# Optimization experiments

Hardware: AMD Instinct MI355X
Metric: run time of the kernel (lower is better)

## Reference

```python
import jax, jax.numpy as jnp
import numpy as np


def setup_inputs() -> dict:
    key = jax.random.key(0)
    k1, _ = jax.random.split(key)
    x = jax.random.normal(k1, (2, 16, 16, 16, 64), dtype=jnp.float32)
    gamma = jnp.ones((1,), dtype=jnp.float32)  # learned scalar (zeros at init; ones to make output nontrivial)
    return {"x": x, "gamma": gamma}


def reference(x, gamma):
    # x: (B, D, H, W, C); faithful to the Keras layer: flatten spatial dims,
    # energy = Q @ Q^T over the N=D*H*W axis, softmax(axis=-1), attn @ Q,
    # then gamma-scaled residual add.
    B, D, H, W, C = x.shape
    N = D * H * W
    q = x.reshape(B, N, C)                            # proj_query (B, N, C)
    energy = jnp.einsum('bnc,bmc->bnm', q, q)          # (B, N, N)
    attn = jax.nn.softmax(energy, axis=-1)
    out = jnp.einsum('bnm,bmc->bnc', attn, q)          # (B, N, C)
    out = out.reshape(B, D, H, W, C)
    return gamma * out + x
```

## Files before the change

### kernel.cpp

```cpp
#include <hip/hip_runtime.h>
#include <hip/hip_bf16.h>
#include <math.h>


#define NN 4096
#define CC 64
#define LOG2E 1.4426950408889634f

typedef __attribute__((ext_vector_type(4))) float f32x4;
typedef __attribute__((ext_vector_type(8))) short bf16x8;
typedef __attribute__((ext_vector_type(4))) short bf16x4;
typedef unsigned short u16;
typedef __attribute__((ext_vector_type(4))) u16 u16x4;

__device__ inline u16 f2bf(float f) {
  union { float f; unsigned u; } v; v.f = f;
  unsigned r = (v.u + 0x7fffu + ((v.u >> 16) & 1u)) >> 16;
  return (u16)r;
}
__device__ inline u16 f2bf_t(float f) {
  union { float f; unsigned u; } v; v.f = f;
  return (u16)(v.u >> 16);
}
__device__ inline float bf2f(short h) {
  union { unsigned u; float f; } v;
  v.u = ((unsigned)(unsigned short)h) << 16;
  return v.f;
}
__device__ inline bf16x8 cvt8(f32x4 a, f32x4 b) {
  bf16x8 r;
  r[0] = (short)f2bf(a[0]); r[1] = (short)f2bf(a[1]);
  r[2] = (short)f2bf(a[2]); r[3] = (short)f2bf(a[3]);
  r[4] = (short)f2bf(b[0]); r[5] = (short)f2bf(b[1]);
  r[6] = (short)f2bf(b[2]); r[7] = (short)f2bf(b[3]);
  return r;
}

__global__ __launch_bounds__(256) void prep_kernel(const float* __restrict__ x,
                                                   u16* __restrict__ Qb,
                                                   u16* __restrict__ Vt) {
  __shared__ u16 t[64][20];
  int b = blockIdx.x >> 8;
  int n0 = (blockIdx.x & 255) << 4;
  const f32x4* x4 = (const f32x4*)(x + ((size_t)b * NN + n0) * CC);
  u16* qb = Qb + ((size_t)b * NN + n0) * CC;
  {
    int idx4 = threadIdx.x;
    int i = idx4 >> 4, cg = idx4 & 15;
    f32x4 v = x4[idx4];
    u16x4 h;
    h[0] = f2bf(v[0]); h[1] = f2bf(v[1]); h[2] = f2bf(v[2]); h[3] = f2bf(v[3]);
    *(u16x4*)(qb + (size_t)i * CC + cg * 4) = h;
    t[cg * 4 + 0][i] = h[0]; t[cg * 4 + 1][i] = h[1];
    t[cg * 4 + 2][i] = h[2]; t[cg * 4 + 3][i] = h[3];
  }
  __syncthreads();
  int kb = n0 >> 6, kw0 = n0 & 63;
  {
    int idx4 = threadIdx.x;
    int c = idx4 >> 2, i4 = (idx4 & 3) * 4;
    u16x4 h = *(const u16x4*)(&t[c][i4]);
    *(u16x4*)(Vt + (((size_t)b * (NN / 64) + kb) * 64 + c) * 64 + kw0 + i4) = h;
  }
}

template <int S>
__global__ __launch_bounds__(256, 2) void attn_split(
    const u16* __restrict__ Qb, const u16* __restrict__ Vt,
    u16* __restrict__ Opart, float* __restrict__ lpart) {
  constexpr int KPS = NN / S;
  constexpr int ITERS = KPS / 64;
  const int w = threadIdx.x >> 6;
  const int lane = threadIdx.x & 63;
  const int quad = lane >> 4, col = lane & 15;
  const int blk = blockIdx.x;
  const int b = blk / (32 * S);
  const int rb = (blk / S) & 31;
  const int s = blk % S;

  __shared__ u16 KT[2][64 * 68];
  __shared__ u16 VT[2][64 * 68];
  __shared__ u16 PB[4][16 * 68];

  const u16* Qbase = Qb + (size_t)b * NN * CC;
  const u16* Vbase = Vt + (size_t)b * NN * CC;
  const int row0 = rb * 128 + w * 32;

  bf16x8 qs0[2], qs1[2];
  float m_i[2][4];
#pragma unroll
  for (int rt = 0; rt < 2; ++rt) {
    const u16* qp = Qbase + (size_t)(row0 + rt * 16 + col) * CC + quad * 8;
    bf16x8 r0 = *(const bf16x8*)qp;
    bf16x8 r1 = *(const bf16x8*)(qp + 32);
    float msum = 0.f;
#pragma unroll
    for (int j = 0; j < 8; ++j) {
      float a0 = bf2f(r0[j]), a1 = bf2f(r1[j]);
      u16 h0 = f2bf(a0 * LOG2E), h1 = f2bf(a1 * LOG2E);
      qs0[rt][j] = (short)h0; qs1[rt][j] = (short)h1;
      msum += bf2f((short)h0) * a0 + bf2f((short)h1) * a1;
    }
    msum += __shfl_xor(msum, 16);
    msum += __shfl_xor(msum, 32);
#pragma unroll
    for (int r = 0; r < 4; ++r) m_i[rt][r] = __shfl(msum, quad * 4 + r);
  }

  f32x4 zero = {0.f, 0.f, 0.f, 0.f};
  f32x4 acc[2][4] = {{zero, zero, zero, zero}, {zero, zero, zero, zero}};
  float l_i[2][4] = {{0.f, 0.f, 0.f, 0.f}, {0.f, 0.f, 0.f, 0.f}};

  const int srow = w * 16 + (lane >> 3);
  const int sj = lane & 7;
  bf16x8 stK0, stK1, stV0, stV1;

  auto issue_loads = [&](int kt0) {
    const u16* ks = Qbase + (size_t)(kt0 + srow) * CC + sj * 8;
    stK0 = *(const bf16x8*)ks;
    stK1 = *(const bf16x8*)(ks + 8 * CC);
    const u16* vs = Vbase + ((size_t)(kt0 >> 6)) * 4096 + srow * 64 + sj * 8;
    stV0 = *(const bf16x8*)vs;
    stV1 = *(const bf16x8*)(vs + 8 * 64);
  };
  auto write_tile = [&](int p) {
    *(bf16x8*)(&KT[p][srow * 68 + sj * 8]) = stK0;
    *(bf16x8*)(&KT[p][(srow + 8) * 68 + sj * 8]) = stK1;
    *(bf16x8*)(&VT[p][srow * 68 + sj * 8]) = stV0;
    *(bf16x8*)(&VT[p][(srow + 8) * 68 + sj * 8]) = stV1;
  };

  issue_loads(s * KPS);
  write_tile(0);
#pragma unroll
  for (int i = 0; i < ITERS; ++i) {
    __syncthreads();
    const int p = i & 1;
    if (i + 1 < ITERS) issue_loads(s * KPS + (i + 1) * 64);
    bf16x8 ka[4], kb_[4], va[4], vb[4];
#pragma unroll
    for (int t = 0; t < 4; ++t) {
      ka[t] = *(const bf16x8*)(&KT[p][(t * 16 + col) * 68 + quad * 8]);
      kb_[t] = *(const bf16x8*)(&KT[p][(t * 16 + col) * 68 + 32 + quad * 8]);
      va[t] = *(const bf16x8*)(&VT[p][(t * 16 + col) * 68 + quad * 8]);
      vb[t] = *(const bf16x8*)(&VT[p][(t * 16 + col) * 68 + 32 + quad * 8]);
    }
#pragma unroll
    for (int rt = 0; rt < 2; ++rt) {
      f32x4 sx[4];
#pragma unroll
      for (int t = 0; t < 4; ++t) {
        sx[t] = __builtin_amdgcn_mfma_f32_16x16x32_bf16(qs0[rt], ka[t], zero, 0, 0, 0);
        sx[t] = __builtin_amdgcn_mfma_f32_16x16x32_bf16(qs1[rt], kb_[t], sx[t], 0, 0, 0);
      }
#pragma unroll
      for (int t = 0; t < 4; ++t) {
#pragma unroll
        for (int r = 0; r < 4; ++r) {
          float pv = exp2f(sx[t][r] - m_i[rt][r]);
          l_i[rt][r] += pv;
          PB[w][(quad * 4 + r) * 68 + t * 16 + col] = f2bf_t(pv);
        }
      }
      bf16x8 pf0 = *(const bf16x8*)(&PB[w][col * 68 + quad * 8]);
      bf16x8 pf1 = *(const bf16x8*)(&PB[w][col * 68 + 32 + quad * 8]);
#pragma unroll
      for (int cg = 0; cg < 4; ++cg) {
        acc[rt][cg] = __builtin_amdgcn_mfma_f32_16x16x32_bf16(pf0, va[cg], acc[rt][cg], 0, 0, 0);
        acc[rt][cg] = __builtin_amdgcn_mfma_f32_16x16x32_bf16(pf1, vb[cg], acc[rt][cg], 0, 0, 0);
      }
    }
    if (i + 1 < ITERS) write_tile(p ^ 1);
  }

#pragma unroll
  for (int rt = 0; rt < 2; ++rt)
#pragma unroll
    for (int r = 0; r < 4; ++r)
#pragma unroll
      for (int off = 1; off < 16; off <<= 1)
        l_i[rt][r] += __shfl_xor(l_i[rt][r], off, 16);

  size_t pbase = (((size_t)b * 32 + rb) * S + s) * 128 * 64;
#pragma unroll
  for (int rt = 0; rt < 2; ++rt) {
#pragma unroll
    for (int r = 0; r < 4; ++r) {
      int lr = w * 32 + rt * 16 + quad * 4 + r;
      size_t o = pbase + (size_t)lr * 64;
      Opart[o + col]      = f2bf(acc[rt][0][r]);
      Opart[o + col + 16] = f2bf(acc[rt][1][r]);
      Opart[o + col + 32] = f2bf(acc[rt][2][r]);
      Opart[o + col + 48] = f2bf(acc[rt][3][r]);
      if (col == 0)
        lpart[(((size_t)b * 32 + rb) * S + s) * 128 + lr] = l_i[rt][r];
    }
  }
}

template <int S>
__global__ __launch_bounds__(256) void epi_kernel(
    const float* __restrict__ x, const float* __restrict__ gamma,
    const u16* __restrict__ Opart, const float* __restrict__ lpart,
    float* __restrict__ out) {
  int t = blockIdx.x * 256 + threadIdx.x;
  int cg = t & 15;
  int n = (t >> 4) & (NN - 1);
  int b = t >> 16;
  int rb = n >> 7, lr = n & 127;
  size_t obase = (((size_t)b * 32 + rb) * S) * 128 * 64 + (size_t)lr * 64 + cg * 4;
  size_t lbase = (((size_t)b * 32 + rb) * S) * 128 + lr;
  f32x4 sO = {0.f, 0.f, 0.f, 0.f};
  float sL = 0.f;
#pragma unroll
  for (int s = 0; s < S; ++s) {
    u16x4 o4 = *(const u16x4*)(Opart + obase + (size_t)s * 128 * 64);
    sL += lpart[lbase + s * 128];
    sO[0] += bf2f((short)o4[0]); sO[1] += bf2f((short)o4[1]);
    sO[2] += bf2f((short)o4[2]); sO[3] += bf2f((short)o4[3]);
  }
  size_t xi = (((size_t)b * NN + n) * CC + cg * 4);
  f32x4 xv = *(const f32x4*)(x + xi);
  float g = gamma[0], inv = 1.f / sL;
  f32x4 ov;
#pragma unroll
  for (int j = 0; j < 4; ++j) ov[j] = g * (sO[j] * inv) + xv[j];
  *(f32x4*)(((float*)out) + xi) = ov;
}

template <int WPB>
__global__ __launch_bounds__(WPB * 64, 4) void attn_fast(
    const float* __restrict__ x, const float* __restrict__ gamma,
    const u16* __restrict__ Qb, const u16* __restrict__ Vt,
    float* __restrict__ out) {
  const int w = threadIdx.x >> 6;
  const int lane = threadIdx.x & 63;
  const int quad = lane >> 4, col = lane & 15;
  const int b = blockIdx.x >> 8;
  const int tile = (blockIdx.x & 255) << 4;

  extern __shared__ char smem[];
  float* Osh = (float*)smem;
  float* lsh = Osh + WPB * 1024;
  u16* pl = (u16*)(lsh + WPB * 16) + w * 2176;

  const size_t xoff = (size_t)b * NN * CC;
  const u16* Qbase = Qb + xoff;
  const u16* Vbase = Vt + xoff;

  bf16x8 qf0 = *(const bf16x8*)(Qbase + (size_t)(tile + col) * CC + quad * 8);
  bf16x8 qf1 = *(const bf16x8*)(Qbase + (size_t)(tile + col) * CC + 32 + quad * 8);

  float msum = 0.f;
#pragma unroll
  for (int j = 0; j < 8; ++j) {
    float a = bf2f(qf0[j]), c = bf2f(qf1[j]);
    msum += a * a + c * c;
  }
  msum += __shfl_xor(msum, 16);
  msum += __shfl_xor(msum, 32);
  float m_i[4];
#pragma unroll
  for (int r = 0; r < 4; ++r) m_i[r] = __shfl(msum, quad * 4 + r);

  f32x4 zero = {0.f, 0.f, 0.f, 0.f};
  f32x4 acc[4] = {zero, zero, zero, zero};
  float l_i[4] = {0.f, 0.f, 0.f, 0.f};

  const int k0 = w * (NN / WPB);
#pragma unroll 2
  for (int kt = k0; kt < k0 + NN / WPB; kt += 64) {
    u16* plc = pl + ((kt >> 6) & 1) * 1088;
    f32x4 sx[4];
#pragma unroll
    for (int t = 0; t < 4; ++t) {
      const u16* kp = Qbase + (size_t)(kt + t * 16 + col) * CC + quad * 8;
      bf16x8 ka = *(const bf16x8*)kp;
      bf16x8 kb = *(const bf16x8*)(kp + 32);
      sx[t] = __builtin_amdgcn_mfma_f32_16x16x32_bf16(qf0, ka, zero, 0, 0, 0);
      sx[t] = __builtin_amdgcn_mfma_f32_16x16x32_bf16(qf1, kb, sx[t], 0, 0, 0);
    }
#pragma unroll
    for (int t = 0; t < 4; ++t) {
#pragma unroll
      for (int r = 0; r < 4; ++r) {
        float p = __expf(sx[t][r] - m_i[r]);
        l_i[r] += p;
        plc[(quad * 4 + r) * 68 + t * 16 + col] = f2bf(p);
      }
    }
    bf16x8 pf0 = *(const bf16x8*)(plc + col * 68 + quad * 8);
    bf16x8 pf1 = *(const bf16x8*)(plc + col * 68 + 32 + quad * 8);
#pragma unroll
    for (int cg = 0; cg < 4; ++cg) {
      const u16* vp = Vbase + (((size_t)(kt >> 6)) * 64 + cg * 16 + col) * 64 + quad * 8;
      bf16x8 v0 = *(const bf16x8*)vp;
      bf16x8 v1 = *(const bf16x8*)(vp + 32);
      acc[cg] = __builtin_amdgcn_mfma_f32_16x16x32_bf16(pf0, v0, acc[cg], 0, 0, 0);
      acc[cg] = __builtin_amdgcn_mfma_f32_16x16x32_bf16(pf1, v1, acc[cg], 0, 0, 0);
    }
  }

#pragma unroll
  for (int r = 0; r < 4; ++r)
#pragma unroll
    for (int off = 1; off < 16; off <<= 1) l_i[r] += __shfl_xor(l_i[r], off, 16);
#pragma unroll
  for (int r = 0; r < 4; ++r) {
    int row = quad * 4 + r;
    Osh[(w * 16 + row) * 64 + col]      = acc[0][r];
    Osh[(w * 16 + row) * 64 + col + 16] = acc[1][r];
    Osh[(w * 16 + row) * 64 + col + 32] = acc[2][r];
    Osh[(w * 16 + row) * 64 + col + 48] = acc[3][r];
    if (col == 0) lsh[w * 16 + row] = l_i[r];
  }
  __syncthreads();

  float g = gamma[0];
  for (int row = w; row < 16; row += WPB) {
    float L = 0.f, val = 0.f;
#pragma unroll
    for (int w2 = 0; w2 < WPB; ++w2) {
      L += lsh[w2 * 16 + row];
      val += Osh[(w2 * 16 + row) * 64 + lane];
    }
    size_t o = xoff + (size_t)(tile + row) * CC + lane;
    out[o] = g * (val / L) + x[o];
  }
}

template <int WPB>
__global__ __launch_bounds__(512) void attn_fb(const float* __restrict__ x,
                                               const float* __restrict__ gamma,
                                               float* __restrict__ out) {
  const int w = threadIdx.x >> 6;
  const int lane = threadIdx.x & 63;
  const int quad = lane >> 4, col = lane & 15;
  const int b = blockIdx.x >> 8;
  const int tile = (blockIdx.x & 255) << 4;

  extern __shared__ char smem[];
  float* Osh = (float*)smem;
  float* msh = Osh + WPB * 1024;
  float* lsh = msh + WPB * 16;
  u16* pl = (u16*)(lsh + WPB * 16) + w * 768;
  u16* vt = (u16*)(lsh + WPB * 16) + WPB * 768 + w * 2176;

  const size_t xoff = (size_t)b * NN * CC;
  const f32x4* x4 = (const f32x4*)(x + xoff);

  bf16x8 qf0, qf1;
  {
    int ri = (tile + col) * 16 + quad * 2;
    qf0 = cvt8(x4[ri], x4[ri + 1]);
    qf1 = cvt8(x4[ri + 8], x4[ri + 9]);
  }
  f32x4 zero = {0.f, 0.f, 0.f, 0.f};
  f32x4 acc0 = zero, acc1 = zero, acc2 = zero, acc3 = zero;
  float m_i[4], l_i[4];
#pragma unroll
  for (int r = 0; r < 4; ++r) { m_i[r] = -1e30f; l_i[r] = 0.f; }

  const int k0 = w * (NN / WPB);
  for (int kt = k0; kt < k0 + NN / WPB; kt += 32) {
    bf16x8 k00, k01, k10, k11;
    {
      int kb = (kt + col) * 16 + quad * 2;
      k00 = cvt8(x4[kb], x4[kb + 1]);
      k01 = cvt8(x4[kb + 8], x4[kb + 9]);
      k10 = cvt8(x4[kb + 256], x4[kb + 257]);
      k11 = cvt8(x4[kb + 264], x4[kb + 265]);
#pragma unroll
      for (int h = 0; h < 2; ++h) {
        bf16x8 va = h ? k10 : k00, vb = h ? k11 : k01;
        int base = (h * 16 + col) * 68 + quad * 8;
        *(bf16x4*)(vt + base) = __builtin_shufflevector(va, va, 0, 1, 2, 3);
        *(bf16x4*)(vt + base + 4) = __builtin_shufflevector(va, va, 4, 5, 6, 7);
        *(bf16x4*)(vt + base + 32) = __builtin_shufflevector(vb, vb, 0, 1, 2, 3);
        *(bf16x4*)(vt + base + 36) = __builtin_shufflevector(vb, vb, 4, 5, 6, 7);
      }
    }
    f32x4 s0 = zero, s1 = zero;
    s0 = __builtin_amdgcn_mfma_f32_16x16x32_bf16(qf0, k00, s0, 0, 0, 0);
    s0 = __builtin_amdgcn_mfma_f32_16x16x32_bf16(qf1, k01, s0, 0, 0, 0);
    s1 = __builtin_amdgcn_mfma_f32_16x16x32_bf16(qf0, k10, s1, 0, 0, 0);
    s1 = __builtin_amdgcn_mfma_f32_16x16x32_bf16(qf1, k11, s1, 0, 0, 0);

    float p0[4], p1[4], alpha[4];
#pragma unroll
    for (int r = 0; r < 4; ++r) {
      float mx = fmaxf(s0[r], s1[r]);
#pragma unroll
      for (int off = 1; off < 16; off <<= 1) mx = fmaxf(mx, __shfl_xor(mx, off, 16));
      float mn = fmaxf(m_i[r], mx);
      alpha[r] = __expf(m_i[r] - mn);
      p0[r] = __expf(s0[r] - mn);
      p1[r] = __expf(s1[r] - mn);
      float rs = p0[r] + p1[r];
#pragma unroll
      for (int off = 1; off < 16; off <<= 1) rs += __shfl_xor(rs, off, 16);
      l_i[r] = l_i[r] * alpha[r] + rs;
      m_i[r] = mn;
    }
#pragma unroll
    for (int r = 0; r < 4; ++r) {
      acc0[r] *= alpha[r]; acc1[r] *= alpha[r];
      acc2[r] *= alpha[r]; acc3[r] *= alpha[r];
    }
#pragma unroll
    for (int r = 0; r < 4; ++r) {
      pl[(quad * 4 + r) * 24 + col] = f2bf(p0[r]);
      pl[384 + (quad * 4 + r) * 24 + col] = f2bf(p1[r]);
    }
    bf16x8 pf = *(const bf16x8*)(pl + (quad >> 1) * 384 + col * 24 + (quad & 1) * 8);

    bf16x8 v0, v1, v2, v3;
#pragma unroll
    for (int j = 0; j < 8; ++j) {
      int rb = (quad * 8 + j) * 68 + col;
      v0[j] = (short)vt[rb];
      v1[j] = (short)vt[rb + 16];
      v2[j] = (short)vt[rb + 32];
      v3[j] = (short)vt[rb + 48];
    }
    acc0 = __builtin_amdgcn_mfma_f32_16x16x32_bf16(pf, v0, acc0, 0, 0, 0);
    acc1 = __builtin_amdgcn_mfma_f32_16x16x32_bf16(pf, v1, acc1, 0, 0, 0);
    acc2 = __builtin_amdgcn_mfma_f32_16x16x32_bf16(pf, v2, acc2, 0, 0, 0);
    acc3 = __builtin_amdgcn_mfma_f32_16x16x32_bf16(pf, v3, acc3, 0, 0, 0);
  }

#pragma unroll
  for (int r = 0; r < 4; ++r) {
    int row = quad * 4 + r;
    Osh[(w * 16 + row) * 64 + col] = acc0[r];
    Osh[(w * 16 + row) * 64 + col + 16] = acc1[r];
    Osh[(w * 16 + row) * 64 + col + 32] = acc2[r];
    Osh[(w * 16 + row) * 64 + col + 48] = acc3[r];
    if (col == 0) { msh[w * 16 + row] = m_i[r]; lsh[w * 16 + row] = l_i[r]; }
  }
  __syncthreads();

  float g = gamma[0];
  for (int row = w; row < 16; row += WPB) {
    float M = -1e30f;
#pragma unroll
    for (int w2 = 0; w2 < WPB; ++w2) M = fmaxf(M, msh[w2 * 16 + row]);
    float L = 0.f, val = 0.f;
#pragma unroll
    for (int w2 = 0; w2 < WPB; ++w2) {
      float e = __expf(msh[w2 * 16 + row] - M);
      L += lsh[w2 * 16 + row] * e;
      val += Osh[(w2 * 16 + row) * 64 + lane] * e;
    }
    size_t o = xoff + (size_t)(tile + row) * CC + lane;
    out[o] = g * (val / L) + x[o];
  }
}

extern "C" void kernel_launch(void* const* d_in, const int* in_sizes, int n_in,
                              void* d_out, int out_size, void* d_ws, size_t ws_size,
                              hipStream_t stream) {
  const float* x = (const float*)d_in[0];
  const float* gamma = (const float*)d_in[1];
  float* out = (float*)d_out;

  constexpr int S = 16;
  constexpr size_t kQV = (size_t)2 * 2 * NN * CC * sizeof(u16);
  constexpr size_t kOp = (size_t)2 * 32 * S * 128 * 64 * sizeof(u16);
  constexpr size_t kLp = (size_t)2 * 32 * S * 128 * sizeof(float);
  if (ws_size >= kQV + kOp + kLp) {
    u16* Qb = (u16*)d_ws;
    u16* Vt = Qb + (size_t)2 * NN * CC;
    u16* Opart = (u16*)((char*)d_ws + kQV);
    float* lpart = (float*)((char*)d_ws + kQV + kOp);
    prep_kernel<<<512, 256, 0, stream>>>(x, Qb, Vt);
    attn_split<S><<<2 * 32 * S, 256, 0, stream>>>(Qb, Vt, Opart, lpart);
    epi_kernel<S><<<(2 * NN * 16) / 256, 256, 0, stream>>>(x, gamma, Opart, lpart, out);
  } else if (ws_size >= kQV) {
    u16* Qb = (u16*)d_ws;
    u16* Vt = Qb + (size_t)2 * NN * CC;
    prep_kernel<<<512, 256, 0, stream>>>(x, Qb, Vt);
    constexpr int SM = 8 * 1024 * 4 + 8 * 16 * 4 + 8 * 2176 * 2;
    attn_fast<8><<<512, 512, SM, stream>>>(x, gamma, Qb, Vt, out);
  } else {
    constexpr int SM4 = 4 * (1024 + 32) * 4 + 4 * 768 * 2 + 4 * 2176 * 2;
    attn_fb<4><<<512, 256, SM4, stream>>>(x, gamma, out);
  }
}
```

Before: 90.09 us.

## Use direct global-to-LDS loads with XOR swizzle and swapped MFMA operands in split attention

Rewrites the split-K attention kernel to load K/V tiles straight into LDS with global_load_lds, replacing the register-staged copies, and uses an XOR-swizzled unpadded LDS layout to avoid bank conflicts. The QK^T MFMA operands are swapped so each lane holds the scores for a single query row. This lets the row-max constant and row sum stay per-lane, and probabilities are packed to bf16 with perm and written as 8-byte stores instead of scalar stores. Blocks are shrunk to 128 threads with 64 query rows each and the key split count is halved, which changes the partial-buffer layout and the epilogue indexing to match.

Result: faster. 83.28 us (-7.6%).

```diff
diff --git a/kernel.cpp b/kernel.cpp
--- a/kernel.cpp
+++ b/kernel.cpp
@@ -12,20 +12,21 @@
 typedef __attribute__((ext_vector_type(4))) short bf16x4;
 typedef unsigned short u16;
 typedef __attribute__((ext_vector_type(4))) u16 u16x4;
+typedef __attribute__((ext_vector_type(2))) unsigned u32x2;
 
 __device__ inline u16 f2bf(float f) {
   union { float f; unsigned u; } v; v.f = f;
   unsigned r = (v.u + 0x7fffu + ((v.u >> 16) & 1u)) >> 16;
   return (u16)r;
 }
-__device__ inline u16 f2bf_t(float f) {
-  union { float f; unsigned u; } v; v.f = f;
-  return (u16)(v.u >> 16);
-}
 __device__ inline float bf2f(short h) {
   union { unsigned u; float f; } v;
   v.u = ((unsigned)(unsigned short)h) << 16;
   return v.f;
+}
+__device__ inline unsigned fbits(float f) {
+  union { float f; unsigned u; } v; v.f = f;
+  return v.u;
 }
 __device__ inline bf16x8 cvt8(f32x4 a, f32x4 b) {
   bf16x8 r;
@@ -65,7 +66,7 @@
 }
 
 template <int S>
-__global__ __launch_bounds__(256, 2) void attn_split(
+__global__ __launch_bounds__(128, 2) void attn_split(
     const u16* __restrict__ Qb, const u16* __restrict__ Vt,
     u16* __restrict__ Opart, float* __restrict__ lpart) {
   constexpr int KPS = NN / S;
@@ -74,20 +75,20 @@
   const int lane = threadIdx.x & 63;
   const int quad = lane >> 4, col = lane & 15;
   const int blk = blockIdx.x;
-  const int b = blk / (32 * S);
-  const int rb = (blk / S) & 31;
+  const int b = blk / (64 * S);
+  const int rb = (blk / S) & 63;
   const int s = blk % S;
 
-  __shared__ u16 KT[2][64 * 68];
-  __shared__ u16 VT[2][64 * 68];
-  __shared__ u16 PB[4][16 * 68];
+  __shared__ u16 KT[2][64 * 64];
+  __shared__ u16 VT[2][64 * 64];
+  __shared__ u16 PB[2][16 * 72];
 
   const u16* Qbase = Qb + (size_t)b * NN * CC;
   const u16* Vbase = Vt + (size_t)b * NN * CC;
-  const int row0 = rb * 128 + w * 32;
+  const int row0 = rb * 64 + w * 32;
 
   bf16x8 qs0[2], qs1[2];
-  float m_i[2][4];
+  float m_sc[2];
 #pragma unroll
   for (int rt = 0; rt < 2; ++rt) {
     const u16* qp = Qbase + (size_t)(row0 + rt * 16 + col) * CC + quad * 8;
@@ -103,87 +104,89 @@
     }
     msum += __shfl_xor(msum, 16);
     msum += __shfl_xor(msum, 32);
-#pragma unroll
-    for (int r = 0; r < 4; ++r) m_i[rt][r] = __shfl(msum, quad * 4 + r);
+    m_sc[rt] = msum;
   }
 
   f32x4 zero = {0.f, 0.f, 0.f, 0.f};
   f32x4 acc[2][4] = {{zero, zero, zero, zero}, {zero, zero, zero, zero}};
-  float l_i[2][4] = {{0.f, 0.f, 0.f, 0.f}, {0.f, 0.f, 0.f, 0.f}};
-
-  const int srow = w * 16 + (lane >> 3);
-  const int sj = lane & 7;
-  bf16x8 stK0, stK1, stV0, stV1;
-
-  auto issue_loads = [&](int kt0) {
-    const u16* ks = Qbase + (size_t)(kt0 + srow) * CC + sj * 8;
-    stK0 = *(const bf16x8*)ks;
-    stK1 = *(const bf16x8*)(ks + 8 * CC);
-    const u16* vs = Vbase + ((size_t)(kt0 >> 6)) * 4096 + srow * 64 + sj * 8;
-    stV0 = *(const bf16x8*)vs;
-    stV1 = *(const bf16x8*)(vs + 8 * 64);
-  };
-  auto write_tile = [&](int p) {
-    *(bf16x8*)(&KT[p][srow * 68 + sj * 8]) = stK0;
-    *(bf16x8*)(&KT[p][(srow + 8) * 68 + sj * 8]) = stK1;
-    *(bf16x8*)(&VT[p][srow * 68 + sj * 8]) = stV0;
-    *(bf16x8*)(&VT[p][(srow + 8) * 68 + sj * 8]) = stV1;
-  };
-
-  issue_loads(s * KPS);
-  write_tile(0);
-#pragma unroll
+  float l_loc[2] = {0.f, 0.f};
+
+  const int kk = lane >> 3;
+  const int sw = (lane & 7) ^ kk;
+  const u16* kptr = Qbase + (size_t)(s * KPS + w * 32 + kk) * CC + sw * 8;
+  const u16* vptr = Vbase + ((size_t)(s * KPS >> 6) * 64 + (w * 32 + kk)) * 64 + sw * 8;
+
+#define STAGE(p, kp, vp)                                                      \
+  {                                                                           \
+    _Pragma("unroll")                                                         \
+    for (int g = 0; g < 4; ++g) {                                             \
+      __builtin_amdgcn_global_load_lds(                                       \
+          (const __attribute__((address_space(1))) unsigned*)((kp) + g * 512),\
+          (__attribute__((address_space(3))) unsigned*)&KT[p][(w * 32 + g * 8) * 64], \
+          16, 0, 0);                                                          \
+      __builtin_amdgcn_global_load_lds(                                       \
+          (const __attribute__((address_space(1))) unsigned*)((vp) + g * 512),\
+          (__attribute__((address_space(3))) unsigned*)&VT[p][(w * 32 + g * 8) * 64], \
+          16, 0, 0);                                                          \
+    }                                                                         \
+  }
+
+  STAGE(0, kptr, vptr)
+#pragma unroll 2
   for (int i = 0; i < ITERS; ++i) {
     __syncthreads();
     const int p = i & 1;
-    if (i + 1 < ITERS) issue_loads(s * KPS + (i + 1) * 64);
+    if (i + 1 < ITERS) STAGE(p ^ 1, kptr + 4096, vptr + 4096)
+    kptr += 4096; vptr += 4096;
+
+    const int cs = col & 7;
     bf16x8 ka[4], kb_[4], va[4], vb[4];
 #pragma unroll
     for (int t = 0; t < 4; ++t) {
-      ka[t] = *(const bf16x8*)(&KT[p][(t * 16 + col) * 68 + quad * 8]);
-      kb_[t] = *(const bf16x8*)(&KT[p][(t * 16 + col) * 68 + 32 + quad * 8]);
-      va[t] = *(const bf16x8*)(&VT[p][(t * 16 + col) * 68 + quad * 8]);
-      vb[t] = *(const bf16x8*)(&VT[p][(t * 16 + col) * 68 + 32 + quad * 8]);
+      ka[t]  = *(const bf16x8*)&KT[p][(t * 16 + col) * 64 + (quad ^ cs) * 8];
+      kb_[t] = *(const bf16x8*)&KT[p][(t * 16 + col) * 64 + ((quad + 4) ^ cs) * 8];
+      va[t]  = *(const bf16x8*)&VT[p][(t * 16 + col) * 64 + (quad ^ cs) * 8];
+      vb[t]  = *(const bf16x8*)&VT[p][(t * 16 + col) * 64 + ((quad + 4) ^ cs) * 8];
     }
 #pragma unroll
     for (int rt = 0; rt < 2; ++rt) {
       f32x4 sx[4];
 #pragma unroll
       for (int t = 0; t < 4; ++t) {
-        sx[t] = __builtin_amdgcn_mfma_f32_16x16x32_bf16(qs0[rt], ka[t], zero, 0, 0, 0);
-        sx[t] = __builtin_amdgcn_mfma_f32_16x16x32_bf16(qs1[rt], kb_[t], sx[t], 0, 0, 0);
+        sx[t] = __builtin_amdgcn_mfma_f32_16x16x32_bf16(ka[t], qs0[rt], zero, 0, 0, 0);
+        sx[t] = __builtin_amdgcn_mfma_f32_16x16x32_bf16(kb_[t], qs1[rt], sx[t], 0, 0, 0);
       }
+      u16* PBw = &PB[w][0];
 #pragma unroll
       for (int t = 0; t < 4; ++t) {
-#pragma unroll
-        for (int r = 0; r < 4; ++r) {
-          float pv = exp2f(sx[t][r] - m_i[rt][r]);
-          l_i[rt][r] += pv;
-          PB[w][(quad * 4 + r) * 68 + t * 16 + col] = f2bf_t(pv);
-        }
+        f32x4 pv;
+#pragma unroll
+        for (int r = 0; r < 4; ++r) pv[r] = exp2f(sx[t][r] - m_sc[rt]);
+        l_loc[rt] += pv[0] + pv[1] + pv[2] + pv[3];
+        u32x2 d;
+        d[0] = __builtin_amdgcn_perm(fbits(pv[1]), fbits(pv[0]), 0x07060302u);
+        d[1] = __builtin_amdgcn_perm(fbits(pv[3]), fbits(pv[2]), 0x07060302u);
+        *(u32x2*)&PBw[col * 72 + t * 16 + quad * 4] = d;
       }
-      bf16x8 pf0 = *(const bf16x8*)(&PB[w][col * 68 + quad * 8]);
-      bf16x8 pf1 = *(const bf16x8*)(&PB[w][col * 68 + 32 + quad * 8]);
+      bf16x8 pf0 = *(const bf16x8*)&PBw[col * 72 + quad * 8];
+      bf16x8 pf1 = *(const bf16x8*)&PBw[col * 72 + 32 + quad * 8];
 #pragma unroll
       for (int cg = 0; cg < 4; ++cg) {
         acc[rt][cg] = __builtin_amdgcn_mfma_f32_16x16x32_bf16(pf0, va[cg], acc[rt][cg], 0, 0, 0);
         acc[rt][cg] = __builtin_amdgcn_mfma_f32_16x16x32_bf16(pf1, vb[cg], acc[rt][cg], 0, 0, 0);
       }
     }
-    if (i + 1 < ITERS) write_tile(p ^ 1);
-  }
-
-#pragma unroll
-  for (int rt = 0; rt < 2; ++rt)
-#pragma unroll
-    for (int r = 0; r < 4; ++r)
-#pragma unroll
-      for (int off = 1; off < 16; off <<= 1)
-        l_i[rt][r] += __shfl_xor(l_i[rt][r], off, 16);
-
-  size_t pbase = (((size_t)b * 32 + rb) * S + s) * 128 * 64;
+  }
+#undef STAGE
+
+  size_t pbase = (((size_t)(b * 64 + rb)) * S + s) * (64 * 64);
+  size_t lbase = (((size_t)(b * 64 + rb)) * S + s) * 64;
 #pragma unroll
   for (int rt = 0; rt < 2; ++rt) {
+    float l = l_loc[rt];
+    l += __shfl_xor(l, 16);
+    l += __shfl_xor(l, 32);
+    if (quad == 0) lpart[lbase + w * 32 + rt * 16 + col] = l;
 #pragma unroll
     for (int r = 0; r < 4; ++r) {
       int lr = w * 32 + rt * 16 + quad * 4 + r;
@@ -192,8 +195,6 @@
       Opart[o + col + 16] = f2bf(acc[rt][1][r]);
       Opart[o + col + 32] = f2bf(acc[rt][2][r]);
       Opart[o + col + 48] = f2bf(acc[rt][3][r]);
-      if (col == 0)
-        lpart[(((size_t)b * 32 + rb) * S + s) * 128 + lr] = l_i[rt][r];
     }
   }
 }
@@ -207,15 +208,15 @@
   int cg = t & 15;
   int n = (t >> 4) & (NN - 1);
   int b = t >> 16;
-  int rb = n >> 7, lr = n & 127;
-  size_t obase = (((size_t)b * 32 + rb) * S) * 128 * 64 + (size_t)lr * 64 + cg * 4;
-  size_t lbase = (((size_t)b * 32 + rb) * S) * 128 + lr;
+  int rb = n >> 6, lr = n & 63;
+  size_t obase = ((size_t)(b * 64 + rb) * S) * 4096 + (size_t)lr * 64 + cg * 4;
+  size_t lbase = ((size_t)(b * 64 + rb) * S) * 64 + lr;
   f32x4 sO = {0.f, 0.f, 0.f, 0.f};
   float sL = 0.f;
 #pragma unroll
   for (int s = 0; s < S; ++s) {
-    u16x4 o4 = *(const u16x4*)(Opart + obase + (size_t)s * 128 * 64);
-    sL += lpart[lbase + s * 128];
+    u16x4 o4 = *(const u16x4*)(Opart + obase + (size_t)s * 4096);
+    sL += lpart[lbase + s * 64];
     sO[0] += bf2f((short)o4[0]); sO[1] += bf2f((short)o4[1]);
     sO[2] += bf2f((short)o4[2]); sO[3] += bf2f((short)o4[3]);
   }
@@ -464,17 +465,17 @@
   const float* gamma = (const float*)d_in[1];
   float* out = (float*)d_out;
 
-  constexpr int S = 16;
+  constexpr int S = 8;
   constexpr size_t kQV = (size_t)2 * 2 * NN * CC * sizeof(u16);
-  constexpr size_t kOp = (size_t)2 * 32 * S * 128 * 64 * sizeof(u16);
-  constexpr size_t kLp = (size_t)2 * 32 * S * 128 * sizeof(float);
+  constexpr size_t kOp = (size_t)2 * 64 * S * 64 * 64 * sizeof(u16);
+  constexpr size_t kLp = (size_t)2 * 64 * S * 64 * sizeof(float);
   if (ws_size >= kQV + kOp + kLp) {
     u16* Qb = (u16*)d_ws;
     u16* Vt = Qb + (size_t)2 * NN * CC;
     u16* Opart = (u16*)((char*)d_ws + kQV);
     float* lpart = (float*)((char*)d_ws + kQV + kOp);
     prep_kernel<<<512, 256, 0, stream>>>(x, Qb, Vt);
-    attn_split<S><<<2 * 32 * S, 256, 0, stream>>>(Qb, Vt, Opart, lpart);
+    attn_split<S><<<2 * 64 * S, 128, 0, stream>>>(Qb, Vt, Opart, lpart);
     epi_kernel<S><<<(2 * NN * 16) / 256, 256, 0, stream>>>(x, gamma, Opart, lpart, out);
   } else if (ws_size >= kQV) {
     u16* Qb = (u16*)d_ws;
```
